# Kernel optimization log

Hardware: AMD Instinct MI355X
Metric: run time of the kernel (lower is better)

Reference implementation:

```python
import jax, jax.numpy as jnp
import numpy as np
from itertools import permutations

B, T, J = 65536, 3, 10
W_ASSIGN = 1.0  # assignments_loss_weight
W_CAT = 1.0     # categorizer_loss_weight


def setup_inputs() -> dict:
    key = jax.random.key(0)
    k1, k2, k3, k4 = jax.random.split(key, 4)
    assignments = jax.random.uniform(k1, (B, T, J, J), dtype=jnp.float32)
    category = jax.random.uniform(k2, (B, T), dtype=jnp.float32)
    assignments_labels = jax.random.uniform(k3, (B, T, J, J), dtype=jnp.float32)
    category_labels = jax.random.uniform(k4, (B, T), dtype=jnp.float32)
    return {
        "assignments": assignments,
        "category": category,
        "assignments_labels": assignments_labels,
        "category_labels": category_labels,
    }


def _bce(p, y):
    # torch.nn.BCELoss clamps log terms at -100
    logp = jnp.clip(jnp.log(p), -100.0, None)
    log1mp = jnp.clip(jnp.log1p(-p), -100.0, None)
    return -(y * logp + (1.0 - y) * log1mp)


def reference(assignments, category, assignments_labels, category_labels):
    t = assignments.shape[1]
    perms = jnp.asarray(list(permutations(range(t))), dtype=jnp.int32)  # [P, T]
    # gather all permutations at once: [B, P, T, J, J]
    gathered = assignments[:, perms]
    # per-(event, perm) mean BCE vs labels broadcast over perm axis -> [B, P]
    losses = _bce(gathered, assignments_labels[:, None]).mean(axis=(2, 3, 4))
    batch_losses = losses.min(axis=1)          # [B]
    best = losses.argmin(axis=1)               # [B], first-min tie-break like torch's strict <
    best_perm = perms[best]                    # [B, T]
    permuted_category = jnp.take_along_axis(category, best_perm, axis=1)  # [B, T]
    assignments_loss = batch_losses.mean()
    category_loss = _bce(permuted_category, category_labels).mean()
    return W_ASSIGN * assignments_loss + W_CAT * category_loss
```

## Files before the change

### kernel.cpp

```cpp
#include <hip/hip_runtime.h>


#define CLIP2 (-144.26950408889634f)
#define LN2   (0.6931471805599453f)

__launch_bounds__(256)
__global__ void hybrid_pass1(const float* __restrict__ assign,
                             const float* __restrict__ cat,
                             const float* __restrict__ assign_lab,
                             const float* __restrict__ cat_lab,
                             float* __restrict__ ws, int B) {
    const int lane = threadIdx.x & 63;
    const int sub  = lane & 31;
    const int b    = (blockIdx.x * blockDim.x + threadIdx.x) >> 5;
    if (b >= B) return;

    const bool act = sub < 25;
    const float* Ab = assign     + (size_t)b * 300;
    const float* Yb = assign_lab + (size_t)b * 300;

    float s1[3]     = {0.f, 0.f, 0.f};
    float dot[3][3] = {{0.f,0.f,0.f},{0.f,0.f,0.f},{0.f,0.f,0.f}};

    if (act) {
        const int o = sub * 4;
        float4 av0 = *(const float4*)(Ab + o);
        float4 av1 = *(const float4*)(Ab + 100 + o);
        float4 av2 = *(const float4*)(Ab + 200 + o);
        float4 yv0 = *(const float4*)(Yb + o);
        float4 yv1 = *(const float4*)(Yb + 100 + o);
        float4 yv2 = *(const float4*)(Yb + 200 + o);

        float a[3][4] = {{av0.x,av0.y,av0.z,av0.w},
                         {av1.x,av1.y,av1.z,av1.w},
                         {av2.x,av2.y,av2.z,av2.w}};
        float y[3][4] = {{yv0.x,yv0.y,yv0.z,yv0.w},
                         {yv1.x,yv1.y,yv1.z,yv1.w},
                         {yv2.x,yv2.y,yv2.z,yv2.w}};

        float d[3][4];
        #pragma unroll
        for (int t = 0; t < 3; ++t) {
            #pragma unroll
            for (int c = 0; c < 4; ++c) {
                float lp = fmaxf(__log2f(a[t][c]),        CLIP2);
                float l1 = fmaxf(__log2f(1.0f - a[t][c]), CLIP2);
                d[t][c] = lp - l1;
                s1[t]  += l1;
            }
        }
        #pragma unroll
        for (int tl = 0; tl < 3; ++tl) {
            #pragma unroll
            for (int ta = 0; ta < 3; ++ta) {
                float acc = 0.f;
                #pragma unroll
                for (int c = 0; c < 4; ++c)
                    acc = fmaf(y[tl][c], d[ta][c], acc);
                dot[tl][ta] = acc;
            }
        }
    }

    float c0=0.f,c1=0.f,c2=0.f,g0=0.f,g1=0.f,g2=0.f;
    if (sub == 0) {
        const float* cb = cat     + (size_t)b * 3;
        const float* gb = cat_lab + (size_t)b * 3;
        c0 = cb[0]; c1 = cb[1]; c2 = cb[2];
        g0 = gb[0]; g1 = gb[1]; g2 = gb[2];
    }

    #pragma unroll
    for (int off = 16; off > 0; off >>= 1) {
        #pragma unroll
        for (int t = 0; t < 3; ++t) s1[t] += __shfl_xor(s1[t], off, 64);
        #pragma unroll
        for (int tl = 0; tl < 3; ++tl)
            #pragma unroll
            for (int ta = 0; ta < 3; ++ta)
                dot[tl][ta] += __shfl_xor(dot[tl][ta], off, 64);
    }

    float local = 0.0f;
    if (sub == 0) {
        float Cm[3][3];
        #pragma unroll
        for (int tl = 0; tl < 3; ++tl)
            #pragma unroll
            for (int ta = 0; ta < 3; ++ta)
                Cm[tl][ta] = -(s1[ta] + dot[tl][ta]);

        const int P0[6] = {0,0,1,1,2,2};
        const int P1[6] = {1,2,0,2,0,1};
        const int P2[6] = {2,1,2,0,1,0};
        float best = Cm[0][0] + Cm[1][1] + Cm[2][2];
        int bp0 = 0, bp1 = 1, bp2 = 2;
        #pragma unroll
        for (int p = 1; p < 6; ++p) {
            float l = Cm[0][P0[p]] + Cm[1][P1[p]] + Cm[2][P2[p]];
            if (l < best) { best = l; bp0 = P0[p]; bp1 = P1[p]; bp2 = P2[p]; }
        }

        float lp0 = fmaxf(__log2f(c0), CLIP2), l10 = fmaxf(__log2f(1.f-c0), CLIP2);
        float lp1 = fmaxf(__log2f(c1), CLIP2), l11 = fmaxf(__log2f(1.f-c1), CLIP2);
        float lp2 = fmaxf(__log2f(c2), CLIP2), l12 = fmaxf(__log2f(1.f-c2), CLIP2);

        float lpa = (bp0==0)?lp0:((bp0==1)?lp1:lp2);
        float l1a = (bp0==0)?l10:((bp0==1)?l11:l12);
        float lpb = (bp1==0)?lp0:((bp1==1)?lp1:lp2);
        float l1b = (bp1==0)?l10:((bp1==1)?l11:l12);
        float lpc = (bp2==0)?lp0:((bp2==1)?lp1:lp2);
        float l1c = (bp2==0)?l10:((bp2==1)?l11:l12);

        float csum = -(g0*lpa + (1.f-g0)*l1a
                     + g1*lpb + (1.f-g1)*l1b
                     + g2*lpc + (1.f-g2)*l1c);

        local = (best * (1.f/300.f) + csum * (1.f/3.f)) * (LN2 / 65536.f);
    }

    __shared__ float sred[8];
    if (sub == 0) sred[threadIdx.x >> 5] = local;
    __syncthreads();
    if (threadIdx.x == 0) {
        float s = 0.f;
        #pragma unroll
        for (int i = 0; i < 8; ++i) s += sred[i];
        ws[blockIdx.x] = s;
    }
}

__launch_bounds__(1024)
__global__ void hybrid_pass2(const float* __restrict__ ws,
                             float* __restrict__ out, int n) {
    float s = 0.f;
    for (int i = threadIdx.x; i < n; i += 1024) s += ws[i];
    #pragma unroll
    for (int off = 32; off > 0; off >>= 1) s += __shfl_xor(s, off, 64);
    __shared__ float sm[16];
    if ((threadIdx.x & 63) == 0) sm[threadIdx.x >> 6] = s;
    __syncthreads();
    if (threadIdx.x == 0) {
        float t = 0.f;
        #pragma unroll
        for (int i = 0; i < 16; ++i) t += sm[i];
        out[0] = t;
    }
}

extern "C" void kernel_launch(void* const* d_in, const int* in_sizes, int n_in,
                              void* d_out, int out_size, void* d_ws, size_t ws_size,
                              hipStream_t stream) {
    const float* assign     = (const float*)d_in[0];
    const float* cat        = (const float*)d_in[1];
    const float* assign_lab = (const float*)d_in[2];
    const float* cat_lab    = (const float*)d_in[3];
    float* out = (float*)d_out;
    float* ws  = (float*)d_ws;

    const int B = in_sizes[0] / 300;
    const int threads = 256;
    const int blocks  = (B * 32 + threads - 1) / threads;

    hybrid_pass1<<<blocks, threads, 0, stream>>>(assign, cat, assign_lab,
                                                 cat_lab, ws, B);
    hybrid_pass2<<<1, 1024, 0, stream>>>(ws, out, blocks);
}
```

Before: 179.1 us.

## Make pass1 grid-stride with double-buffered register prefetch of next event

Each 32-lane half-wave now handles four events in a grid-stride loop, loading the next event's assignments, labels and category into a second register set while computing the current one. The s1 term is folded into the per-permutation dot accumulators, so fewer values go through the shuffle reduction, and the comparison is flipped to a max on the un-negated cost. The aim is to hide global load latency and cut block count and partial sums, at the cost of more registers and a smaller grid (2048 blocks).

```diff
diff --git a/kernel.cpp b/kernel.cpp
--- a/kernel.cpp
+++ b/kernel.cpp
@@ -4,106 +4,95 @@
 #define CLIP2 (-144.26950408889634f)
 #define LN2   (0.6931471805599453f)
 
-__launch_bounds__(256)
-__global__ void hybrid_pass1(const float* __restrict__ assign,
-                             const float* __restrict__ cat,
-                             const float* __restrict__ assign_lab,
-                             const float* __restrict__ cat_lab,
-                             float* __restrict__ ws, int B) {
-    const int lane = threadIdx.x & 63;
-    const int sub  = lane & 31;
-    const int b    = (blockIdx.x * blockDim.x + threadIdx.x) >> 5;
-    if (b >= B) return;
+__device__ __forceinline__ void load_b(const float* __restrict__ assign,
+                                       const float* __restrict__ assign_lab,
+                                       const float* __restrict__ cat,
+                                       const float* __restrict__ cat_lab,
+                                       int b, bool act, int o, int sub,
+                                       float4 (&A)[3], float4 (&Y)[3],
+                                       float (&cb)[3], float (&gb)[3]) {
+    if (act) {
+        const float* Ab = assign     + (size_t)b * 300 + o;
+        const float* Yb = assign_lab + (size_t)b * 300 + o;
+        A[0] = *(const float4*)(Ab);
+        A[1] = *(const float4*)(Ab + 100);
+        A[2] = *(const float4*)(Ab + 200);
+        Y[0] = *(const float4*)(Yb);
+        Y[1] = *(const float4*)(Yb + 100);
+        Y[2] = *(const float4*)(Yb + 200);
+    }
+    if (sub == 0) {
+        const float* cp = cat     + (size_t)b * 3;
+        const float* gp = cat_lab + (size_t)b * 3;
+        cb[0] = cp[0]; cb[1] = cp[1]; cb[2] = cp[2];
+        gb[0] = gp[0]; gb[1] = gp[1]; gb[2] = gp[2];
+    }
+}
 
-    const bool act = sub < 25;
-    const float* Ab = assign     + (size_t)b * 300;
-    const float* Yb = assign_lab + (size_t)b * 300;
-
-    float s1[3]     = {0.f, 0.f, 0.f};
-    float dot[3][3] = {{0.f,0.f,0.f},{0.f,0.f,0.f},{0.f,0.f,0.f}};
+__device__ __forceinline__ void compute_b(bool act, int sub,
+                                          const float4 (&A)[3],
+                                          const float4 (&Y)[3],
+                                          const float (&cb)[3],
+                                          const float (&gb)[3],
+                                          float& lsum) {
+    float e[3][3] = {{0.f,0.f,0.f},{0.f,0.f,0.f},{0.f,0.f,0.f}};
 
     if (act) {
-        const int o = sub * 4;
-        float4 av0 = *(const float4*)(Ab + o);
-        float4 av1 = *(const float4*)(Ab + 100 + o);
-        float4 av2 = *(const float4*)(Ab + 200 + o);
-        float4 yv0 = *(const float4*)(Yb + o);
-        float4 yv1 = *(const float4*)(Yb + 100 + o);
-        float4 yv2 = *(const float4*)(Yb + 200 + o);
-
-        float a[3][4] = {{av0.x,av0.y,av0.z,av0.w},
-                         {av1.x,av1.y,av1.z,av1.w},
-                         {av2.x,av2.y,av2.z,av2.w}};
-        float y[3][4] = {{yv0.x,yv0.y,yv0.z,yv0.w},
-                         {yv1.x,yv1.y,yv1.z,yv1.w},
-                         {yv2.x,yv2.y,yv2.z,yv2.w}};
-
+        float a[3][4] = {{A[0].x,A[0].y,A[0].z,A[0].w},
+                         {A[1].x,A[1].y,A[1].z,A[1].w},
+                         {A[2].x,A[2].y,A[2].z,A[2].w}};
+        float y[3][4] = {{Y[0].x,Y[0].y,Y[0].z,Y[0].w},
+                         {Y[1].x,Y[1].y,Y[1].z,Y[1].w},
+                         {Y[2].x,Y[2].y,Y[2].z,Y[2].w}};
         float d[3][4];
+        float s1p[3] = {0.f, 0.f, 0.f};
         #pragma unroll
         for (int t = 0; t < 3; ++t) {
             #pragma unroll
             for (int c = 0; c < 4; ++c) {
-                float lp = fmaxf(__log2f(a[t][c]),        CLIP2);
+                float lp = fmaxf(__log2f(a[t][c]),       CLIP2);
                 float l1 = fmaxf(__log2f(1.0f - a[t][c]), CLIP2);
                 d[t][c] = lp - l1;
-                s1[t]  += l1;
+                s1p[t] += l1;
             }
         }
         #pragma unroll
         for (int tl = 0; tl < 3; ++tl) {
             #pragma unroll
             for (int ta = 0; ta < 3; ++ta) {
-                float acc = 0.f;
+                float acc = s1p[ta];
                 #pragma unroll
                 for (int c = 0; c < 4; ++c)
                     acc = fmaf(y[tl][c], d[ta][c], acc);
-                dot[tl][ta] = acc;
+                e[tl][ta] = acc;
             }
         }
-    }
-
-    float c0=0.f,c1=0.f,c2=0.f,g0=0.f,g1=0.f,g2=0.f;
-    if (sub == 0) {
-        const float* cb = cat     + (size_t)b * 3;
-        const float* gb = cat_lab + (size_t)b * 3;
-        c0 = cb[0]; c1 = cb[1]; c2 = cb[2];
-        g0 = gb[0]; g1 = gb[1]; g2 = gb[2];
     }
 
     #pragma unroll
     for (int off = 16; off > 0; off >>= 1) {
         #pragma unroll
-        for (int t = 0; t < 3; ++t) s1[t] += __shfl_xor(s1[t], off, 64);
-        #pragma unroll
         for (int tl = 0; tl < 3; ++tl)
             #pragma unroll
             for (int ta = 0; ta < 3; ++ta)
-                dot[tl][ta] += __shfl_xor(dot[tl][ta], off, 64);
+                e[tl][ta] += __shfl_xor(e[tl][ta], off, 64);
     }
 
-    float local = 0.0f;
     if (sub == 0) {
-        float Cm[3][3];
-        #pragma unroll
-        for (int tl = 0; tl < 3; ++tl)
-            #pragma unroll
-            for (int ta = 0; ta < 3; ++ta)
-                Cm[tl][ta] = -(s1[ta] + dot[tl][ta]);
-
         const int P0[6] = {0,0,1,1,2,2};
         const int P1[6] = {1,2,0,2,0,1};
         const int P2[6] = {2,1,2,0,1,0};
-        float best = Cm[0][0] + Cm[1][1] + Cm[2][2];
+        float best = e[0][0] + e[1][1] + e[2][2];
         int bp0 = 0, bp1 = 1, bp2 = 2;
         #pragma unroll
         for (int p = 1; p < 6; ++p) {
-            float l = Cm[0][P0[p]] + Cm[1][P1[p]] + Cm[2][P2[p]];
-            if (l < best) { best = l; bp0 = P0[p]; bp1 = P1[p]; bp2 = P2[p]; }
+            float l = e[0][P0[p]] + e[1][P1[p]] + e[2][P2[p]];
+            if (l > best) { best = l; bp0 = P0[p]; bp1 = P1[p]; bp2 = P2[p]; }
         }
 
-        float lp0 = fmaxf(__log2f(c0), CLIP2), l10 = fmaxf(__log2f(1.f-c0), CLIP2);
-        float lp1 = fmaxf(__log2f(c1), CLIP2), l11 = fmaxf(__log2f(1.f-c1), CLIP2);
-        float lp2 = fmaxf(__log2f(c2), CLIP2), l12 = fmaxf(__log2f(1.f-c2), CLIP2);
+        float lp0 = fmaxf(__log2f(cb[0]), CLIP2), l10 = fmaxf(__log2f(1.f-cb[0]), CLIP2);
+        float lp1 = fmaxf(__log2f(cb[1]), CLIP2), l11 = fmaxf(__log2f(1.f-cb[1]), CLIP2);
+        float lp2 = fmaxf(__log2f(cb[2]), CLIP2), l12 = fmaxf(__log2f(1.f-cb[2]), CLIP2);
 
         float lpa = (bp0==0)?lp0:((bp0==1)?lp1:lp2);
         float l1a = (bp0==0)?l10:((bp0==1)?l11:l12);
@@ -112,12 +101,49 @@
         float lpc = (bp2==0)?lp0:((bp2==1)?lp1:lp2);
         float l1c = (bp2==0)?l10:((bp2==1)?l11:l12);
 
-        float csum = -(g0*lpa + (1.f-g0)*l1a
-                     + g1*lpb + (1.f-g1)*l1b
-                     + g2*lpc + (1.f-g2)*l1c);
+        float csum = -(gb[0]*lpa + (1.f-gb[0])*l1a
+                     + gb[1]*lpb + (1.f-gb[1])*l1b
+                     + gb[2]*lpc + (1.f-gb[2])*l1c);
 
-        local = (best * (1.f/300.f) + csum * (1.f/3.f)) * (LN2 / 65536.f);
+        lsum += best * (-1.f/300.f) + csum * (1.f/3.f);
     }
+}
+
+__launch_bounds__(256)
+__global__ void hybrid_pass1(const float* __restrict__ assign,
+                             const float* __restrict__ cat,
+                             const float* __restrict__ assign_lab,
+                             const float* __restrict__ cat_lab,
+                             float* __restrict__ ws, int B) {
+    const int sub = threadIdx.x & 31;
+    const int hid = (blockIdx.x * blockDim.x + threadIdx.x) >> 5;
+    const int nh  = (gridDim.x * blockDim.x) >> 5;
+    const bool act = sub < 25;
+    const int o = sub * 4;
+
+    float4 A0[3], Y0[3], A1[3], Y1[3];
+    float  c0[3], g0[3], c1[3], g1[3];
+    float  lsum = 0.f;
+
+    int b = hid;
+    if (b < B) {
+        load_b(assign, assign_lab, cat, cat_lab, b, act, o, sub, A0, Y0, c0, g0);
+        while (true) {
+            int b1 = b + nh;
+            if (b1 < B)
+                load_b(assign, assign_lab, cat, cat_lab, b1, act, o, sub, A1, Y1, c1, g1);
+            compute_b(act, sub, A0, Y0, c0, g0, lsum);
+            if (b1 >= B) break;
+            int b2 = b1 + nh;
+            if (b2 < B)
+                load_b(assign, assign_lab, cat, cat_lab, b2, act, o, sub, A0, Y0, c0, g0);
+            compute_b(act, sub, A1, Y1, c1, g1, lsum);
+            if (b2 >= B) break;
+            b = b2;
+        }
+    }
+
+    float local = (sub == 0) ? lsum * (LN2 / 65536.f) : 0.f;
 
     __shared__ float sred[8];
     if (sub == 0) sred[threadIdx.x >> 5] = local;
@@ -159,10 +185,12 @@
     float* ws  = (float*)d_ws;
 
     const int B = in_sizes[0] / 300;
-    const int threads = 256;
-    const int blocks  = (B * 32 + threads - 1) / threads;
 
-    hybrid_pass1<<<blocks, threads, 0, stream>>>(assign, cat, assign_lab,
-                                                 cat_lab, ws, B);
+    const int ITERS  = 4;
+    const int halves = (B + ITERS - 1) / ITERS;
+    const int blocks = (halves + 7) / 8;
+
+    hybrid_pass1<<<blocks, 256, 0, stream>>>(assign, cat, assign_lab,
+                                             cat_lab, ws, B);
     hybrid_pass2<<<1, 1024, 0, stream>>>(ws, out, blocks);
 }
```

Measured after the change: 181.1 us. About the same (+1.1%).

## Process each batch event with 4 threads looping over chunks instead of 32

Applied to the files above, without the earlier changes.

Each event was handled by 32 lanes, with 7 of them idle; now 4 lanes each loop over 16-float chunks, accumulating dot products and log sums in registers. This removes idle lanes and cuts the cross-lane shuffle reduction from five rounds over twelve values to two rounds over nine. The sign is folded so that the best permutation is the maximum. In exchange, each thread does serial work with more registers and fewer waves in flight, and loads within a wave are strided per event, which may reduce memory-level parallelism on a bandwidth-bound kernel.

```diff
diff --git a/kernel.cpp b/kernel.cpp
--- a/kernel.cpp
+++ b/kernel.cpp
@@ -10,123 +10,119 @@
                              const float* __restrict__ assign_lab,
                              const float* __restrict__ cat_lab,
                              float* __restrict__ ws, int B) {
-    const int lane = threadIdx.x & 63;
-    const int sub  = lane & 31;
-    const int b    = (blockIdx.x * blockDim.x + threadIdx.x) >> 5;
-    if (b >= B) return;
+    const int tid = blockIdx.x * blockDim.x + threadIdx.x;
+    const int b   = tid >> 2;
+    const int q   = threadIdx.x & 3;
 
-    const bool act = sub < 25;
-    const float* Ab = assign     + (size_t)b * 300;
-    const float* Yb = assign_lab + (size_t)b * 300;
+    float lsum = 0.f;
 
-    float s1[3]     = {0.f, 0.f, 0.f};
-    float dot[3][3] = {{0.f,0.f,0.f},{0.f,0.f,0.f},{0.f,0.f,0.f}};
+    if (b < B) {
+        const float* Abq = assign     + (size_t)b * 300 + 4 * q;
+        const float* Ybq = assign_lab + (size_t)b * 300 + 4 * q;
 
-    if (act) {
-        const int o = sub * 4;
-        float4 av0 = *(const float4*)(Ab + o);
-        float4 av1 = *(const float4*)(Ab + 100 + o);
-        float4 av2 = *(const float4*)(Ab + 200 + o);
-        float4 yv0 = *(const float4*)(Yb + o);
-        float4 yv1 = *(const float4*)(Yb + 100 + o);
-        float4 yv2 = *(const float4*)(Yb + 200 + o);
+        const float* cp = cat     + (size_t)b * 3;
+        const float* gp = cat_lab + (size_t)b * 3;
+        float cb0 = cp[0], cb1 = cp[1], cb2 = cp[2];
+        float gb0 = gp[0], gb1 = gp[1], gb2 = gp[2];
 
-        float a[3][4] = {{av0.x,av0.y,av0.z,av0.w},
-                         {av1.x,av1.y,av1.z,av1.w},
-                         {av2.x,av2.y,av2.z,av2.w}};
-        float y[3][4] = {{yv0.x,yv0.y,yv0.z,yv0.w},
-                         {yv1.x,yv1.y,yv1.z,yv1.w},
-                         {yv2.x,yv2.y,yv2.z,yv2.w}};
+        float dacc[3][3] = {{0.f,0.f,0.f},{0.f,0.f,0.f},{0.f,0.f,0.f}};
+        float s1a[3]     = {0.f, 0.f, 0.f};
 
-        float d[3][4];
+        auto do_chunk = [&](const float* Ap, const float* Yp) {
+            float4 av[3], yv[3];
+            #pragma unroll
+            for (int t = 0; t < 3; ++t) {
+                av[t] = *(const float4*)(Ap + t * 100);
+                yv[t] = *(const float4*)(Yp + t * 100);
+            }
+            float d[3][4];
+            #pragma unroll
+            for (int t = 0; t < 3; ++t) {
+                float a[4] = {av[t].x, av[t].y, av[t].z, av[t].w};
+                #pragma unroll
+                for (int c = 0; c < 4; ++c) {
+                    float lp = fmaxf(__log2f(a[c]),        CLIP2);
+                    float l1 = fmaxf(__log2f(1.0f - a[c]), CLIP2);
+                    d[t][c] = lp - l1;
+                    s1a[t] += l1;
+                }
+            }
+            #pragma unroll
+            for (int tl = 0; tl < 3; ++tl) {
+                float y[4] = {yv[tl].x, yv[tl].y, yv[tl].z, yv[tl].w};
+                #pragma unroll
+                for (int ta = 0; ta < 3; ++ta) {
+                    float acc = dacc[tl][ta];
+                    #pragma unroll
+                    for (int c = 0; c < 4; ++c)
+                        acc = fmaf(y[c], d[ta][c], acc);
+                    dacc[tl][ta] = acc;
+                }
+            }
+        };
+
         #pragma unroll
-        for (int t = 0; t < 3; ++t) {
-            #pragma unroll
-            for (int c = 0; c < 4; ++c) {
-                float lp = fmaxf(__log2f(a[t][c]),        CLIP2);
-                float l1 = fmaxf(__log2f(1.0f - a[t][c]), CLIP2);
-                d[t][c] = lp - l1;
-                s1[t]  += l1;
-            }
-        }
-        #pragma unroll
-        for (int tl = 0; tl < 3; ++tl) {
-            #pragma unroll
-            for (int ta = 0; ta < 3; ++ta) {
-                float acc = 0.f;
-                #pragma unroll
-                for (int c = 0; c < 4; ++c)
-                    acc = fmaf(y[tl][c], d[ta][c], acc);
-                dot[tl][ta] = acc;
-            }
-        }
-    }
+        for (int k = 0; k < 6; ++k)
+            do_chunk(Abq + 16 * k, Ybq + 16 * k);
+        if (q == 0)
+            do_chunk(Abq + 96, Ybq + 96);
 
-    float c0=0.f,c1=0.f,c2=0.f,g0=0.f,g1=0.f,g2=0.f;
-    if (sub == 0) {
-        const float* cb = cat     + (size_t)b * 3;
-        const float* gb = cat_lab + (size_t)b * 3;
-        c0 = cb[0]; c1 = cb[1]; c2 = cb[2];
-        g0 = gb[0]; g1 = gb[1]; g2 = gb[2];
-    }
-
-    #pragma unroll
-    for (int off = 16; off > 0; off >>= 1) {
-        #pragma unroll
-        for (int t = 0; t < 3; ++t) s1[t] += __shfl_xor(s1[t], off, 64);
+        float e[3][3];
         #pragma unroll
         for (int tl = 0; tl < 3; ++tl)
             #pragma unroll
             for (int ta = 0; ta < 3; ++ta)
-                dot[tl][ta] += __shfl_xor(dot[tl][ta], off, 64);
+                e[tl][ta] = dacc[tl][ta] + s1a[ta];
+
+        #pragma unroll
+        for (int off = 1; off <= 2; off <<= 1)
+            #pragma unroll
+            for (int tl = 0; tl < 3; ++tl)
+                #pragma unroll
+                for (int ta = 0; ta < 3; ++ta)
+                    e[tl][ta] += __shfl_xor(e[tl][ta], off, 64);
+
+        if (q == 0) {
+            const int P0[6] = {0,0,1,1,2,2};
+            const int P1[6] = {1,2,0,2,0,1};
+            const int P2[6] = {2,1,2,0,1,0};
+            float best = e[0][0] + e[1][1] + e[2][2];
+            int bp0 = 0, bp1 = 1, bp2 = 2;
+            #pragma unroll
+            for (int p = 1; p < 6; ++p) {
+                float l = e[0][P0[p]] + e[1][P1[p]] + e[2][P2[p]];
+                if (l > best) { best = l; bp0 = P0[p]; bp1 = P1[p]; bp2 = P2[p]; }
+            }
+
+            float lp0 = fmaxf(__log2f(cb0), CLIP2), l10 = fmaxf(__log2f(1.f-cb0), CLIP2);
+            float lp1 = fmaxf(__log2f(cb1), CLIP2), l11 = fmaxf(__log2f(1.f-cb1), CLIP2);
+            float lp2 = fmaxf(__log2f(cb2), CLIP2), l12 = fmaxf(__log2f(1.f-cb2), CLIP2);
+
+            float lpa = (bp0==0)?lp0:((bp0==1)?lp1:lp2);
+            float l1a = (bp0==0)?l10:((bp0==1)?l11:l12);
+            float lpb = (bp1==0)?lp0:((bp1==1)?lp1:lp2);
+            float l1b = (bp1==0)?l10:((bp1==1)?l11:l12);
+            float lpc = (bp2==0)?lp0:((bp2==1)?lp1:lp2);
+            float l1c = (bp2==0)?l10:((bp2==1)?l11:l12);
+
+            float csum = -(gb0*lpa + (1.f-gb0)*l1a
+                         + gb1*lpb + (1.f-gb1)*l1b
+                         + gb2*lpc + (1.f-gb2)*l1c);
+
+            lsum = best * (-1.f/300.f) + csum * (1.f/3.f);
+        }
     }
 
-    float local = 0.0f;
-    if (sub == 0) {
-        float Cm[3][3];
-        #pragma unroll
-        for (int tl = 0; tl < 3; ++tl)
-            #pragma unroll
-            for (int ta = 0; ta < 3; ++ta)
-                Cm[tl][ta] = -(s1[ta] + dot[tl][ta]);
+    #pragma unroll
+    for (int off = 4; off <= 32; off <<= 1)
+        lsum += __shfl_xor(lsum, off, 64);
 
-        const int P0[6] = {0,0,1,1,2,2};
-        const int P1[6] = {1,2,0,2,0,1};
-        const int P2[6] = {2,1,2,0,1,0};
-        float best = Cm[0][0] + Cm[1][1] + Cm[2][2];
-        int bp0 = 0, bp1 = 1, bp2 = 2;
-        #pragma unroll
-        for (int p = 1; p < 6; ++p) {
-            float l = Cm[0][P0[p]] + Cm[1][P1[p]] + Cm[2][P2[p]];
-            if (l < best) { best = l; bp0 = P0[p]; bp1 = P1[p]; bp2 = P2[p]; }
-        }
-
-        float lp0 = fmaxf(__log2f(c0), CLIP2), l10 = fmaxf(__log2f(1.f-c0), CLIP2);
-        float lp1 = fmaxf(__log2f(c1), CLIP2), l11 = fmaxf(__log2f(1.f-c1), CLIP2);
-        float lp2 = fmaxf(__log2f(c2), CLIP2), l12 = fmaxf(__log2f(1.f-c2), CLIP2);
-
-        float lpa = (bp0==0)?lp0:((bp0==1)?lp1:lp2);
-        float l1a = (bp0==0)?l10:((bp0==1)?l11:l12);
-        float lpb = (bp1==0)?lp0:((bp1==1)?lp1:lp2);
-        float l1b = (bp1==0)?l10:((bp1==1)?l11:l12);
-        float lpc = (bp2==0)?lp0:((bp2==1)?lp1:lp2);
-        float l1c = (bp2==0)?l10:((bp2==1)?l11:l12);
-
-        float csum = -(g0*lpa + (1.f-g0)*l1a
-                     + g1*lpb + (1.f-g1)*l1b
-                     + g2*lpc + (1.f-g2)*l1c);
-
-        local = (best * (1.f/300.f) + csum * (1.f/3.f)) * (LN2 / 65536.f);
-    }
-
-    __shared__ float sred[8];
-    if (sub == 0) sred[threadIdx.x >> 5] = local;
+    __shared__ float sred[4];
+    if ((threadIdx.x & 63) == 0) sred[threadIdx.x >> 6] = lsum;
     __syncthreads();
     if (threadIdx.x == 0) {
-        float s = 0.f;
-        #pragma unroll
-        for (int i = 0; i < 8; ++i) s += sred[i];
-        ws[blockIdx.x] = s;
+        float s = (sred[0] + sred[1]) + (sred[2] + sred[3]);
+        ws[blockIdx.x] = s * (LN2 / 65536.f);
     }
 }
 
@@ -159,10 +155,9 @@
     float* ws  = (float*)d_ws;
 
     const int B = in_sizes[0] / 300;
-    const int threads = 256;
-    const int blocks  = (B * 32 + threads - 1) / threads;
+    const int blocks = (B * 4 + 255) / 256;
 
-    hybrid_pass1<<<blocks, threads, 0, stream>>>(assign, cat, assign_lab,
-                                                 cat_lab, ws, B);
+    hybrid_pass1<<<blocks, 256, 0, stream>>>(assign, cat, assign_lab,
+                                             cat_lab, ws, B);
     hybrid_pass2<<<1, 1024, 0, stream>>>(ws, out, blocks);
 }
```

Result: slower. 184.0 us (+2.7%).
